# Optimization experiments

Hardware: AMD Instinct MI355X
Metric: run time of the kernel (lower is better)

Reference implementation:

```python
import jax, jax.numpy as jnp
import numpy as np

D_MODEL = 1024
N_HEADS = 16
D_FF = 4096
N_EXPERTS = 8
TOP_K = 2
BATCH = 2
SEQ = 2048
LN_EPS = 1e-5


def setup_inputs() -> dict:
    key = jax.random.key(0)
    ks = jax.random.split(key, 16)

    def w(k, shape, fan_in):
        return (jax.random.normal(k, shape, jnp.float32) / np.sqrt(fan_in)).astype(jnp.float32)

    D, F, E = D_MODEL, D_FF, N_EXPERTS
    return {
        "x": jax.random.normal(ks[0], (BATCH, SEQ, D), jnp.float32),
        "Wq": w(ks[1], (D, D), D), "bq": jnp.zeros((D,), jnp.float32),
        "Wk": w(ks[2], (D, D), D), "bk": jnp.zeros((D,), jnp.float32),
        "Wv": w(ks[3], (D, D), D), "bv": jnp.zeros((D,), jnp.float32),
        "Wo": w(ks[4], (D, D), D), "bo": jnp.zeros((D,), jnp.float32),
        "ln1_g": jnp.ones((D,), jnp.float32), "ln1_b": jnp.zeros((D,), jnp.float32),
        "gate_w": w(ks[5], (D, E), D), "gate_b": jnp.zeros((E,), jnp.float32),
        "W1": w(ks[6], (E, D, F), D), "b1": jnp.zeros((E, F), jnp.float32),
        "W2": w(ks[7], (E, F, D), F), "b2": jnp.zeros((E, D), jnp.float32),
        "ln3_g": jnp.ones((D,), jnp.float32), "ln3_b": jnp.zeros((D,), jnp.float32),
    }


def _layernorm(h, g, b):
    m = h.mean(-1, keepdims=True)
    v = ((h - m) ** 2).mean(-1, keepdims=True)
    return (h - m) * jax.lax.rsqrt(v + LN_EPS) * g + b


def _mha(x, Wq, bq, Wk, bk, Wv, bv, Wo, bo):
    B, S, D = x.shape
    H = N_HEADS
    dk = D // H
    q = (x @ Wq + bq).reshape(B, S, H, dk)
    k = (x @ Wk + bk).reshape(B, S, H, dk)
    v = (x @ Wv + bv).reshape(B, S, H, dk)
    scores = jnp.einsum("bqhd,bkhd->bhqk", q, k) / np.sqrt(dk)
    attn = jax.nn.softmax(scores, axis=-1)
    ctx = jnp.einsum("bhqk,bkhd->bqhd", attn, v).reshape(B, S, D)
    return ctx @ Wo + bo


def _moe(x, gate_w, gate_b, W1, b1, W2, b2):
    B, S, D = x.shape
    E = N_EXPERTS
    xf = x.reshape(-1, D)  # [T, D]
    logits = xf @ gate_w + gate_b  # [T, E]
    sc, idx = jax.lax.top_k(logits, TOP_K)
    sc = jax.nn.softmax(sc, axis=-1)  # softmax over the top-k scores only
    # combine weights per (token, expert): sum_k score_k * onehot(idx_k)
    comb = (jax.nn.one_hot(idx, E, dtype=xf.dtype) * sc[..., None]).sum(axis=1)  # [T, E]
    h = jnp.einsum("td,edf->tef", xf, W1) + b1  # [T, E, F]
    even = (jnp.arange(E) % 2 == 0)[None, :, None]
    a = jnp.where(even, jax.nn.gelu(h, approximate=False), jax.nn.silu(h))
    y = jnp.einsum("tef,efd->ted", a, W2) + b2  # [T, E, D]
    out = jnp.einsum("ted,te->td", y, comb)
    return out.reshape(B, S, D)


def reference(x, Wq, bq, Wk, bk, Wv, bv, Wo, bo, ln1_g, ln1_b,
              gate_w, gate_b, W1, b1, W2, b2, ln3_g, ln3_b):
    attn_out = _mha(x, Wq, bq, Wk, bk, Wv, bv, Wo, bo)
    x1 = _layernorm(x + attn_out, ln1_g, ln1_b)
    moe_out = _moe(x1, gate_w, gate_b, W1, b1, W2, b2)  # dropout: eval mode = identity
    return _layernorm(x1 + moe_out, ln3_g, ln3_b)
```

## Files before the change

kernel.cpp:

```cpp
#include <hip/hip_runtime.h>


typedef __attribute__((ext_vector_type(8))) short bf16x8;
typedef __attribute__((ext_vector_type(4))) float f32x4;

#define T_TOK 4096
#define DMODEL 1024
#define DFF 4096
#define NEXP 8
#define SEQ 2048
#define NSLOT 8192
#define NSLOT_PAD (8192+256)
#define LDS_STRIDE 72

__device__ __forceinline__ ushort f2b(float f) {
  union { float f; unsigned u; } v; v.f = f;
  unsigned r = (v.u + 0x7FFFu + ((v.u >> 16) & 1u)) >> 16;
  return (ushort)r;
}
__device__ __forceinline__ float b2f(ushort u) {
  union { unsigned u; float f; } v; v.u = ((unsigned)u) << 16; return v.f;
}


__global__ __launch_bounds__(256) void cvt_bf16(const float* __restrict__ in,
                                                ushort* __restrict__ out, long n,
                                                int* __restrict__ cnt) {
  if (blockIdx.x == 0 && threadIdx.x < 16) cnt[threadIdx.x] = 0;
  long i = ((long)blockIdx.x * 256 + threadIdx.x) * 4;
  if (i >= n) return;
  float4 v = *(const float4*)(in + i);
  ushort4 o; o.x = f2b(v.x); o.y = f2b(v.y); o.z = f2b(v.z); o.w = f2b(v.w);
  *(ushort4*)(out + i) = o;
}

__global__ __launch_bounds__(256) void wtrans(const float* __restrict__ in,
                                              ushort* __restrict__ out, int R, int C) {
  __shared__ float tile[64][65];
  long base = (long)blockIdx.z * R * C;
  int r0 = blockIdx.y * 64, c0 = blockIdx.x * 64;
  int t = threadIdx.x;
  int tr = t >> 4, tc = (t & 15) * 4;
#pragma unroll
  for (int i = 0; i < 4; i++) {
    float4 v = *(const float4*)(in + base + (long)(r0 + tr + i * 16) * C + c0 + tc);
    tile[tr + i * 16][tc + 0] = v.x; tile[tr + i * 16][tc + 1] = v.y;
    tile[tr + i * 16][tc + 2] = v.z; tile[tr + i * 16][tc + 3] = v.w;
  }
  __syncthreads();
#pragma unroll
  for (int i = 0; i < 4; i++) {
    int c = tr + i * 16, r = tc;
    ushort4 o;
    o.x = f2b(tile[r + 0][c]); o.y = f2b(tile[r + 1][c]);
    o.z = f2b(tile[r + 2][c]); o.w = f2b(tile[r + 3][c]);
    *(ushort4*)(out + base + (long)(c0 + c) * R + r0 + r) = o;
  }
}

__global__ __launch_bounds__(256) void vtrans(const ushort* __restrict__ Vb,
                                              ushort* __restrict__ Vt) {
  __shared__ ushort tile[64 * 72];
  int s0 = blockIdx.x * 64, h = blockIdx.y, b = blockIdx.z;
  int t = threadIdx.x;
  int chunk = t & 7;
#pragma unroll
  for (int rep = 0; rep < 2; rep++) {
    int row = (t >> 3) + rep * 32;
    *(uint4*)(tile + row * 72 + chunk * 8) =
        *(const uint4*)(Vb + (long)(b * SEQ + s0 + row) * DMODEL + h * 64 + chunk * 8);
  }
  __syncthreads();
#pragma unroll
  for (int rep = 0; rep < 2; rep++) {
    int idx = rep * 256 + t; int d = idx >> 3; int sc = (idx & 7) * 8;
    union { ushort u[8]; uint4 v; } tmp;
#pragma unroll
    for (int j = 0; j < 8; j++) tmp.u[j] = tile[(sc + j) * 72 + d];
    *(uint4*)(Vt + ((long)(b * 16 + h) * 64 + d) * SEQ + s0 + sc) = tmp.v;
  }
}


__device__ __forceinline__ void mainloop64(
    const ushort* a0, const ushort* a1, const ushort* a2, const ushort* a3,
    const ushort* b0, const ushort* b1, const ushort* b2, const ushort* b3,
    ushort* As, ushort* Bs, int K,
    int wm, int wn, int quad, int l15, f32x4 acc[4][4]) {
  const int t = threadIdx.x;
  const int rA = t >> 3, c8 = (t & 7) * 8;
  for (int k0 = 0; k0 < K; k0 += 64) {
    __syncthreads();
    *(uint4*)(As + (rA +  0) * LDS_STRIDE + c8) = *(const uint4*)(a0 + k0);
    *(uint4*)(As + (rA + 32) * LDS_STRIDE + c8) = *(const uint4*)(a1 + k0);
    *(uint4*)(As + (rA + 64) * LDS_STRIDE + c8) = *(const uint4*)(a2 + k0);
    *(uint4*)(As + (rA + 96) * LDS_STRIDE + c8) = *(const uint4*)(a3 + k0);
    *(uint4*)(Bs + (rA +  0) * LDS_STRIDE + c8) = *(const uint4*)(b0 + k0);
    *(uint4*)(Bs + (rA + 32) * LDS_STRIDE + c8) = *(const uint4*)(b1 + k0);
    *(uint4*)(Bs + (rA + 64) * LDS_STRIDE + c8) = *(const uint4*)(b2 + k0);
    *(uint4*)(Bs + (rA + 96) * LDS_STRIDE + c8) = *(const uint4*)(b3 + k0);
    __syncthreads();
#pragma unroll
    for (int kk = 0; kk < 64; kk += 32) {
      bf16x8 af[4], bfr[4];
#pragma unroll
      for (int i = 0; i < 4; i++)
        af[i] = *(const bf16x8*)(As + (wm + i * 16 + l15) * LDS_STRIDE + kk + quad * 8);
#pragma unroll
      for (int i = 0; i < 4; i++)
        bfr[i] = *(const bf16x8*)(Bs + (wn + i * 16 + l15) * LDS_STRIDE + kk + quad * 8);
#pragma unroll
      for (int mi = 0; mi < 4; mi++)
#pragma unroll
        for (int ni = 0; ni < 4; ni++)
          acc[mi][ni] = __builtin_amdgcn_mfma_f32_16x16x32_bf16(af[mi], bfr[ni], acc[mi][ni], 0, 0, 0);
    }
  }
}

__global__ __launch_bounds__(256, 2) void gemm_qkv(
    const ushort* __restrict__ A,
    const ushort* __restrict__ BtQ, const ushort* __restrict__ BtK, const ushort* __restrict__ BtV,
    const float* __restrict__ bq, const float* __restrict__ bk, const float* __restrict__ bv,
    ushort* __restrict__ oq, ushort* __restrict__ ok, ushort* __restrict__ ov) {
  __shared__ ushort As[128 * LDS_STRIDE], Bs[128 * LDS_STRIDE];
  int z = blockIdx.z;
  const ushort* Bt = (z == 0) ? BtQ : (z == 1) ? BtK : BtV;
  const float* bias = (z == 0) ? bq : (z == 1) ? bk : bv;
  ushort* outp = (z == 0) ? oq : (z == 1) ? ok : ov;
  float scale = (z == 0) ? 0.125f : 1.0f;
  const int m0 = blockIdx.y * 128, n0 = blockIdx.x * 128;
  const int t = threadIdx.x, w = t >> 6, lane = t & 63, quad = lane >> 4, l15 = lane & 15;
  const int wm = (w >> 1) * 64, wn = (w & 1) * 64;
  const int rA = t >> 3, c8 = (t & 7) * 8;
  const ushort* a0 = A + (long)(m0 + rA) * DMODEL + c8;
  const ushort* b0 = Bt + (long)(n0 + rA) * DMODEL + c8;
  f32x4 acc[4][4];
  f32x4 zv = {0.f, 0.f, 0.f, 0.f};
  for (int i = 0; i < 4; i++) for (int j = 0; j < 4; j++) acc[i][j] = zv;
  mainloop64(a0, a0 + 32 * DMODEL, a0 + 64 * DMODEL, a0 + 96 * DMODEL,
             b0, b0 + 32 * DMODEL, b0 + 64 * DMODEL, b0 + 96 * DMODEL,
             As, Bs, DMODEL, wm, wn, quad, l15, acc);
#pragma unroll
  for (int mi = 0; mi < 4; mi++)
#pragma unroll
    for (int ni = 0; ni < 4; ni++) {
      int row = m0 + wm + mi * 16 + quad * 4;
      int col = n0 + wn + ni * 16 + l15;
      float bb = bias[col];
#pragma unroll
      for (int r = 0; r < 4; r++)
        outp[(long)(row + r) * DMODEL + col] = f2b((acc[mi][ni][r] + bb) * scale);
    }
}

__global__ __launch_bounds__(256, 2) void gemm_oproj(
    const ushort* __restrict__ A, const ushort* __restrict__ Bt,
    const float* __restrict__ bias, const float* __restrict__ resid,
    float* __restrict__ outf) {
  __shared__ ushort As[128 * LDS_STRIDE], Bs[128 * LDS_STRIDE];
  const int m0 = blockIdx.y * 128, n0 = blockIdx.x * 128;
  const int t = threadIdx.x, w = t >> 6, lane = t & 63, quad = lane >> 4, l15 = lane & 15;
  const int wm = (w >> 1) * 64, wn = (w & 1) * 64;
  const int rA = t >> 3, c8 = (t & 7) * 8;
  const ushort* a0 = A + (long)(m0 + rA) * DMODEL + c8;
  const ushort* b0 = Bt + (long)(n0 + rA) * DMODEL + c8;
  f32x4 acc[4][4];
  f32x4 zv = {0.f, 0.f, 0.f, 0.f};
  for (int i = 0; i < 4; i++) for (int j = 0; j < 4; j++) acc[i][j] = zv;
  mainloop64(a0, a0 + 32 * DMODEL, a0 + 64 * DMODEL, a0 + 96 * DMODEL,
             b0, b0 + 32 * DMODEL, b0 + 64 * DMODEL, b0 + 96 * DMODEL,
             As, Bs, DMODEL, wm, wn, quad, l15, acc);
#pragma unroll
  for (int mi = 0; mi < 4; mi++)
#pragma unroll
    for (int ni = 0; ni < 4; ni++) {
      int row = m0 + wm + mi * 16 + quad * 4;
      int col = n0 + wn + ni * 16 + l15;
      float bb = bias[col];
#pragma unroll
      for (int r = 0; r < 4; r++) {
        long idx = (long)(row + r) * DMODEL + col;
        outf[idx] = acc[mi][ni][r] + bb + resid[idx];
      }
    }
}

__global__ __launch_bounds__(256, 2) void gemm_moe(
    int mode, const ushort* __restrict__ Abase, const int* __restrict__ slot_token,
    const ushort* __restrict__ WT, const float* __restrict__ biasE,
    ushort* __restrict__ outp, int K, int N,
    const int* __restrict__ tab_e, const int* __restrict__ tab_r0,
    const int* __restrict__ tab_end, const int* __restrict__ nmb) {
  int mb = blockIdx.y;
  if (mb >= *nmb) return;
  __shared__ ushort As[128 * LDS_STRIDE], Bs[128 * LDS_STRIDE];
  int e = tab_e[mb], r0 = tab_r0[mb], rend = tab_end[mb];
  const int t = threadIdx.x, w = t >> 6, lane = t & 63, quad = lane >> 4, l15 = lane & 15;
  const int wm = (w >> 1) * 64, wn = (w & 1) * 64;
  const int rA = t >> 3, c8 = (t & 7) * 8;
  const int n0 = blockIdx.x * 128;
  const ushort* ap[4];
#pragma unroll
  for (int j = 0; j < 4; j++) {
    int r = r0 + rA + 32 * j;
    if (mode == 2) {
      int ci = r < rend ? r : rend - 1;
      ap[j] = Abase + (long)slot_token[ci] * K + c8;
    } else {
      ap[j] = Abase + (long)r * K + c8;
    }
  }
  const ushort* Bt = WT + (long)e * K * N;
  const ushort* b0 = Bt + (long)(n0 + rA) * K + c8;
  f32x4 acc[4][4];
  f32x4 zv = {0.f, 0.f, 0.f, 0.f};
  for (int i = 0; i < 4; i++) for (int j = 0; j < 4; j++) acc[i][j] = zv;
  mainloop64(ap[0], ap[1], ap[2], ap[3],
             b0, b0 + (long)32 * K, b0 + (long)64 * K, b0 + (long)96 * K,
             As, Bs, K, wm, wn, quad, l15, acc);
  const float* bb = biasE + (long)e * N;
  bool odd = (e & 1) != 0;
#pragma unroll
  for (int mi = 0; mi < 4; mi++)
#pragma unroll
    for (int ni = 0; ni < 4; ni++) {
      int col = n0 + wn + ni * 16 + l15;
      float bv = bb[col];
#pragma unroll
      for (int r = 0; r < 4; r++) {
        int slot = r0 + wm + mi * 16 + quad * 4 + r;
        if (slot < rend) {
          float v = acc[mi][ni][r] + bv;
          if (mode == 2)
            v = odd ? (v / (1.f + __expf(-v)))
                    : (0.5f * v * (1.f + erff(v * 0.70710678118f)));
          outp[(long)slot * N + col] = f2b(v);
        }
      }
    }
}

__global__ __launch_bounds__(256, 2) void flash_attn(
    const ushort* __restrict__ Qb, const ushort* __restrict__ Kb,
    const ushort* __restrict__ Vt, ushort* __restrict__ ctx) {
  __shared__ ushort QP[128 * 72];
  __shared__ ushort Ks[64 * 72];
  __shared__ ushort Vs[64 * 72];
  const int t = threadIdx.x, w = t >> 6, lane = t & 63, quad = lane >> 4, l15 = lane & 15;
  const int q0 = blockIdx.x * 128, bh = blockIdx.y, b = bh >> 4, h = bh & 15;
  {
    int chunk = t & 7, hcol = h * 64 + chunk * 8;
#pragma unroll
    for (int rep = 0; rep < 4; rep++) {
      int row = (t >> 3) + rep * 32;
      *(uint4*)(QP + row * 72 + chunk * 8) =
          *(const uint4*)(Qb + (long)(b * SEQ + q0 + row) * DMODEL + hcol);
    }
  }
  __syncthreads();
  bf16x8 qf[2][2];
#pragma unroll
  for (int rt = 0; rt < 2; rt++)
#pragma unroll
    for (int kc = 0; kc < 2; kc++)
      qf[rt][kc] = *(const bf16x8*)(QP + (w * 32 + rt * 16 + l15) * 72 + kc * 32 + quad * 8);

  f32x4 O[2][4];
  f32x4 zv = {0.f, 0.f, 0.f, 0.f};
  float m_r[2][4], l_r[2][4];
#pragma unroll
  for (int rt = 0; rt < 2; rt++)
#pragma unroll
    for (int i = 0; i < 4; i++) { O[rt][i] = zv; m_r[rt][i] = -1e30f; l_r[rt][i] = 0.f; }

  for (int kv0 = 0; kv0 < SEQ; kv0 += 64) {
    __syncthreads();
    {
      int chunk = t & 7, hcol = h * 64 + chunk * 8;
#pragma unroll
      for (int rep = 0; rep < 2; rep++) {
        int row = (t >> 3) + rep * 32;
        *(uint4*)(Ks + row * 72 + chunk * 8) =
            *(const uint4*)(Kb + (long)(b * SEQ + kv0 + row) * DMODEL + hcol);
        *(uint4*)(Vs + row * 72 + chunk * 8) =
            *(const uint4*)(Vt + ((long)bh * 64 + row) * SEQ + kv0 + chunk * 8);
      }
    }
    __syncthreads();
    f32x4 S[2][4];
#pragma unroll
    for (int ct = 0; ct < 4; ct++) {
      bf16x8 kf0 = *(const bf16x8*)(Ks + (ct * 16 + l15) * 72 + quad * 8);
      bf16x8 kf1 = *(const bf16x8*)(Ks + (ct * 16 + l15) * 72 + 32 + quad * 8);
#pragma unroll
      for (int rt = 0; rt < 2; rt++) {
        f32x4 s = zv;
        s = __builtin_amdgcn_mfma_f32_16x16x32_bf16(qf[rt][0], kf0, s, 0, 0, 0);
        s = __builtin_amdgcn_mfma_f32_16x16x32_bf16(qf[rt][1], kf1, s, 0, 0, 0);
        S[rt][ct] = s;
      }
    }
#pragma unroll
    for (int rt = 0; rt < 2; rt++) {
#pragma unroll
      for (int r = 0; r < 4; r++) {
        float mx = fmaxf(fmaxf(S[rt][0][r], S[rt][1][r]), fmaxf(S[rt][2][r], S[rt][3][r]));
        mx = fmaxf(mx, __shfl_xor(mx, 1));
        mx = fmaxf(mx, __shfl_xor(mx, 2));
        mx = fmaxf(mx, __shfl_xor(mx, 4));
        mx = fmaxf(mx, __shfl_xor(mx, 8));
        float nm = fmaxf(m_r[rt][r], mx);
        float alpha = __expf(m_r[rt][r] - nm);
        m_r[rt][r] = nm;
        float p0 = __expf(S[rt][0][r] - nm), p1 = __expf(S[rt][1][r] - nm);
        float p2 = __expf(S[rt][2][r] - nm), p3 = __expf(S[rt][3][r] - nm);
        float rs = p0 + p1 + p2 + p3;
        rs += __shfl_xor(rs, 1); rs += __shfl_xor(rs, 2);
        rs += __shfl_xor(rs, 4); rs += __shfl_xor(rs, 8);
        l_r[rt][r] = l_r[rt][r] * alpha + rs;
#pragma unroll
        for (int dt = 0; dt < 4; dt++) O[rt][dt][r] *= alpha;
        int prow = (w * 32 + rt * 16 + quad * 4 + r) * 72;
        QP[prow + 0 * 16 + l15] = f2b(p0);
        QP[prow + 1 * 16 + l15] = f2b(p1);
        QP[prow + 2 * 16 + l15] = f2b(p2);
        QP[prow + 3 * 16 + l15] = f2b(p3);
      }
    }
    bf16x8 pf[2][2];
#pragma unroll
    for (int rt = 0; rt < 2; rt++)
#pragma unroll
      for (int ks = 0; ks < 2; ks++)
        pf[rt][ks] = *(const bf16x8*)(QP + (w * 32 + rt * 16 + l15) * 72 + ks * 32 + quad * 8);
#pragma unroll
    for (int dt = 0; dt < 4; dt++) {
      bf16x8 vf0 = *(const bf16x8*)(Vs + (dt * 16 + l15) * 72 + quad * 8);
      bf16x8 vf1 = *(const bf16x8*)(Vs + (dt * 16 + l15) * 72 + 32 + quad * 8);
#pragma unroll
      for (int rt = 0; rt < 2; rt++) {
        O[rt][dt] = __builtin_amdgcn_mfma_f32_16x16x32_bf16(pf[rt][0], vf0, O[rt][dt], 0, 0, 0);
        O[rt][dt] = __builtin_amdgcn_mfma_f32_16x16x32_bf16(pf[rt][1], vf1, O[rt][dt], 0, 0, 0);
      }
    }
  }
#pragma unroll
  for (int rt = 0; rt < 2; rt++)
#pragma unroll
    for (int r = 0; r < 4; r++) {
      float inv = 1.f / l_r[rt][r];
      int row = b * SEQ + q0 + w * 32 + rt * 16 + quad * 4 + r;
#pragma unroll
      for (int dt = 0; dt < 4; dt++)
        ctx[(long)row * DMODEL + h * 64 + dt * 16 + l15] = f2b(O[rt][dt][r] * inv);
    }
}


__device__ __forceinline__ float block_sum(float v, float* red) {
#pragma unroll
  for (int off = 32; off; off >>= 1) v += __shfl_down(v, off);
  int w = threadIdx.x >> 6;
  __syncthreads();
  if ((threadIdx.x & 63) == 0) red[w] = v;
  __syncthreads();
  return red[0] + red[1] + red[2] + red[3];
}

__global__ __launch_bounds__(256) void ln1_gate(const float* __restrict__ in,
    const float* __restrict__ g, const float* __restrict__ bb,
    const float* __restrict__ gw, const float* __restrict__ gb,
    float* __restrict__ outf, ushort* __restrict__ outh,
    int* __restrict__ top2i, float* __restrict__ top2s, int* __restrict__ cnt) {
  __shared__ float red[4];
  __shared__ float red8[4][8];
  long row = blockIdx.x;
  int t = threadIdx.x, w = t >> 6, lane = t & 63;
  float4 v = *(const float4*)(in + row * DMODEL + t * 4);
  float s = block_sum(v.x + v.y + v.z + v.w, red);
  float mean = s * (1.0f / DMODEL);
  float d0 = v.x - mean, d1 = v.y - mean, d2 = v.z - mean, d3 = v.w - mean;
  float sq = block_sum(d0 * d0 + d1 * d1 + d2 * d2 + d3 * d3, red);
  float rstd = rsqrtf(sq * (1.0f / DMODEL) + 1e-5f);
  float4 gg = *(const float4*)(g + t * 4);
  float4 bv = *(const float4*)(bb + t * 4);
  float o0 = d0 * rstd * gg.x + bv.x, o1 = d1 * rstd * gg.y + bv.y;
  float o2 = d2 * rstd * gg.z + bv.z, o3 = d3 * rstd * gg.w + bv.w;
  float4 of; of.x = o0; of.y = o1; of.z = o2; of.w = o3;
  *(float4*)(outf + row * DMODEL + t * 4) = of;
  ushort4 oh; oh.x = f2b(o0); oh.y = f2b(o1); oh.z = f2b(o2); oh.w = f2b(o3);
  *(ushort4*)(outh + row * DMODEL + t * 4) = oh;
  float a[8];
  {
    const float* gr = gw + (long)(t * 4) * 8;
    float4 w0 = *(const float4*)(gr +  0), w1 = *(const float4*)(gr +  4);
    float4 w2 = *(const float4*)(gr +  8), w3 = *(const float4*)(gr + 12);
    float4 w4 = *(const float4*)(gr + 16), w5 = *(const float4*)(gr + 20);
    float4 w6 = *(const float4*)(gr + 24), w7 = *(const float4*)(gr + 28);
    a[0] = o0 * w0.x + o1 * w2.x + o2 * w4.x + o3 * w6.x;
    a[1] = o0 * w0.y + o1 * w2.y + o2 * w4.y + o3 * w6.y;
    a[2] = o0 * w0.z + o1 * w2.z + o2 * w4.z + o3 * w6.z;
    a[3] = o0 * w0.w + o1 * w2.w + o2 * w4.w + o3 * w6.w;
    a[4] = o0 * w1.x + o1 * w3.x + o2 * w5.x + o3 * w7.x;
    a[5] = o0 * w1.y + o1 * w3.y + o2 * w5.y + o3 * w7.y;
    a[6] = o0 * w1.z + o1 * w3.z + o2 * w5.z + o3 * w7.z;
    a[7] = o0 * w1.w + o1 * w3.w + o2 * w5.w + o3 * w7.w;
  }
#pragma unroll
  for (int off = 32; off; off >>= 1)
#pragma unroll
    for (int e = 0; e < 8; e++) a[e] += __shfl_down(a[e], off);
  if (lane == 0) {
#pragma unroll
    for (int e = 0; e < 8; e++) red8[w][e] = a[e];
  }
  __syncthreads();
  if (t == 0) {
    float L[8];
#pragma unroll
    for (int e = 0; e < 8; e++)
      L[e] = red8[0][e] + red8[1][e] + red8[2][e] + red8[3][e] + gb[e];
    int e0 = 0; float v0 = L[0];
#pragma unroll
    for (int e = 1; e < 8; e++) if (L[e] > v0) { v0 = L[e]; e0 = e; }
    int e1 = -1; float v1 = -1e30f;
#pragma unroll
    for (int e = 0; e < 8; e++) if (e != e0 && L[e] > v1) { v1 = L[e]; e1 = e; }
    float q = __expf(v1 - v0);
    float inv = 1.f / (1.f + q);
    top2i[2 * row] = e0; top2i[2 * row + 1] = e1;
    top2s[2 * row] = inv; top2s[2 * row + 1] = q * inv;
    atomicAdd(&cnt[e0], 1); atomicAdd(&cnt[e1], 1);
  }
}

__global__ void build_tables(const int* __restrict__ cnt, int* __restrict__ off,
                             int* __restrict__ tab_e, int* __restrict__ tab_r0,
                             int* __restrict__ tab_end, int* __restrict__ nmb) {
  if (threadIdx.x == 0 && blockIdx.x == 0) {
    int o = 0, m = 0;
    for (int e = 0; e < NEXP; e++) {
      off[e] = o;
      int c = cnt[e];
      for (int j = 0; j * 128 < c; j++) { tab_e[m] = e; tab_r0[m] = o + j * 128; tab_end[m] = o + c; m++; }
      o += c;
    }
    off[NEXP] = o;
    *nmb = m;
  }
}

__global__ __launch_bounds__(256) void scatter_slots(const int* __restrict__ top2i,
    const float* __restrict__ top2s, const int* __restrict__ off, int* __restrict__ fill,
    int* __restrict__ slot_token, float* __restrict__ slot_scale, int* __restrict__ pos) {
  int t = blockIdx.x * 256 + threadIdx.x;
  if (t >= T_TOK) return;
#pragma unroll
  for (int k = 0; k < 2; k++) {
    int e = top2i[2 * t + k];
    int p = off[e] + atomicAdd(&fill[e], 1);
    slot_token[p] = t;
    slot_scale[p] = top2s[2 * t + k];
    pos[2 * t + k] = p;
  }
}

__global__ __launch_bounds__(256) void combine_ln3(const float* __restrict__ x1,
    const ushort* __restrict__ ybuf, const int* __restrict__ pos,
    const float* __restrict__ sscale, const float* __restrict__ g,
    const float* __restrict__ bb, float* __restrict__ outp) {
  __shared__ float red[4];
  long row = blockIdx.x;
  int t = threadIdx.x;
  int p0 = pos[2 * row], p1 = pos[2 * row + 1];
  float s0 = sscale[p0], s1 = sscale[p1];
  float4 xv = *(const float4*)(x1 + row * DMODEL + t * 4);
  ushort4 y0 = *(const ushort4*)(ybuf + (long)p0 * DMODEL + t * 4);
  ushort4 y1 = *(const ushort4*)(ybuf + (long)p1 * DMODEL + t * 4);
  float v0 = xv.x + s0 * b2f(y0.x) + s1 * b2f(y1.x);
  float v1 = xv.y + s0 * b2f(y0.y) + s1 * b2f(y1.y);
  float v2 = xv.z + s0 * b2f(y0.z) + s1 * b2f(y1.z);
  float v3 = xv.w + s0 * b2f(y0.w) + s1 * b2f(y1.w);
  float s = block_sum(v0 + v1 + v2 + v3, red);
  float mean = s * (1.0f / DMODEL);
  float d0 = v0 - mean, d1 = v1 - mean, d2 = v2 - mean, d3 = v3 - mean;
  float sq = block_sum(d0 * d0 + d1 * d1 + d2 * d2 + d3 * d3, red);
  float rstd = rsqrtf(sq * (1.0f / DMODEL) + 1e-5f);
  float4 gg = *(const float4*)(g + t * 4);
  float4 bv = *(const float4*)(bb + t * 4);
  float4 of;
  of.x = d0 * rstd * gg.x + bv.x; of.y = d1 * rstd * gg.y + bv.y;
  of.z = d2 * rstd * gg.z + bv.z; of.w = d3 * rstd * gg.w + bv.w;
  *(float4*)(outp + row * DMODEL + t * 4) = of;
}


extern "C" void kernel_launch(void* const* d_in, const int* in_sizes, int n_in,
                              void* d_out, int out_size, void* d_ws, size_t ws_size,
                              hipStream_t stream) {
  (void)in_sizes; (void)n_in; (void)out_size;
  const float* x    = (const float*)d_in[0];
  const float* Wq   = (const float*)d_in[1];
  const float* bq   = (const float*)d_in[2];
  const float* Wk   = (const float*)d_in[3];
  const float* bk   = (const float*)d_in[4];
  const float* Wv   = (const float*)d_in[5];
  const float* bv   = (const float*)d_in[6];
  const float* Wo   = (const float*)d_in[7];
  const float* bo   = (const float*)d_in[8];
  const float* ln1g = (const float*)d_in[9];
  const float* ln1b = (const float*)d_in[10];
  const float* gw   = (const float*)d_in[11];
  const float* gb   = (const float*)d_in[12];
  const float* W1   = (const float*)d_in[13];
  const float* b1   = (const float*)d_in[14];
  const float* W2   = (const float*)d_in[15];
  const float* b2   = (const float*)d_in[16];
  const float* ln3g = (const float*)d_in[17];
  const float* ln3b = (const float*)d_in[18];
  float* outp = (float*)d_out;

  char* ws = (char*)d_ws;
  size_t o = 0;
  auto alloc = [&](size_t b) { size_t r = o; o = (o + b + 255) & ~(size_t)255; return r; };
  const long T = T_TOK, D = DMODEL, F = DFF;
  size_t wqT_o = alloc(D * D * 2), wkT_o = alloc(D * D * 2);
  size_t wvT_o = alloc(D * D * 2), woT_o = alloc(D * D * 2);
  size_t w1T_o = alloc((size_t)NEXP * D * F * 2);
  size_t w2T_o = alloc((size_t)NEXP * D * F * 2);
  size_t xb_o  = alloc(T * D * 2);
  size_t x1f_o = alloc(T * D * 4);
  size_t x1b_o = alloc(T * D * 2);
  size_t yb_o  = alloc((size_t)NSLOT * D * 2);
  size_t ab_o  = alloc((size_t)NSLOT_PAD * F * 2);
  size_t cnt_o = alloc(64);
  size_t off_o = alloc(64);
  size_t nmb_o = alloc(16);
  size_t tabe_o = alloc(80 * 4), tabr_o = alloc(80 * 4), tabn_o = alloc(80 * 4);
  size_t t2i_o = alloc((size_t)NSLOT * 4), t2s_o = alloc((size_t)NSLOT * 4);
  size_t st_o = alloc((size_t)NSLOT * 4), ss_o = alloc((size_t)NSLOT * 4);
  size_t pos_o = alloc((size_t)NSLOT * 4);
  if (o > ws_size) return;

  ushort* wqT = (ushort*)(ws + wqT_o); ushort* wkT = (ushort*)(ws + wkT_o);
  ushort* wvT = (ushort*)(ws + wvT_o); ushort* woT = (ushort*)(ws + woT_o);
  ushort* w1T = (ushort*)(ws + w1T_o); ushort* w2T = (ushort*)(ws + w2T_o);
  ushort* xb  = (ushort*)(ws + xb_o);
  float*  x1f = (float*)(ws + x1f_o);
  ushort* x1b = (ushort*)(ws + x1b_o);
  ushort* ybuf = (ushort*)(ws + yb_o);
  ushort* abuf = (ushort*)(ws + ab_o);
  ushort* qb = abuf;
  ushort* kb = qb + T * D;
  ushort* vb = kb + T * D;
  ushort* vt = vb + T * D;
  ushort* ctx = vt + T * D;
  int* cnt = (int*)(ws + cnt_o); int* fill = cnt + 8;
  int* offe = (int*)(ws + off_o);
  int* nmb = (int*)(ws + nmb_o);
  int* tab_e = (int*)(ws + tabe_o); int* tab_r0 = (int*)(ws + tabr_o);
  int* tab_end = (int*)(ws + tabn_o);
  int* top2i = (int*)(ws + t2i_o); float* top2s = (float*)(ws + t2s_o);
  int* slot_token = (int*)(ws + st_o); float* slot_scale = (float*)(ws + ss_o);
  int* pos = (int*)(ws + pos_o);

  hipLaunchKernelGGL(cvt_bf16, dim3((T * D) / 1024), dim3(256), 0, stream, x, xb, T * D, cnt);
  hipLaunchKernelGGL(wtrans, dim3(16, 16, 1), dim3(256), 0, stream, Wq, wqT, (int)D, (int)D);
  hipLaunchKernelGGL(wtrans, dim3(16, 16, 1), dim3(256), 0, stream, Wk, wkT, (int)D, (int)D);
  hipLaunchKernelGGL(wtrans, dim3(16, 16, 1), dim3(256), 0, stream, Wv, wvT, (int)D, (int)D);
  hipLaunchKernelGGL(wtrans, dim3(16, 16, 1), dim3(256), 0, stream, Wo, woT, (int)D, (int)D);
  hipLaunchKernelGGL(wtrans, dim3(64, 16, 8), dim3(256), 0, stream, W1, w1T, (int)D, (int)F);
  hipLaunchKernelGGL(wtrans, dim3(16, 64, 8), dim3(256), 0, stream, W2, w2T, (int)F, (int)D);
  hipLaunchKernelGGL(gemm_qkv, dim3(8, 32, 3), dim3(256), 0, stream,
                     xb, wqT, wkT, wvT, bq, bk, bv, qb, kb, vb);
  hipLaunchKernelGGL(vtrans, dim3(32, 16, 2), dim3(256), 0, stream, vb, vt);
  hipLaunchKernelGGL(flash_attn, dim3(16, 32), dim3(256), 0, stream, qb, kb, vt, ctx);
  hipLaunchKernelGGL(gemm_oproj, dim3(8, 32), dim3(256), 0, stream, ctx, woT, bo, x, x1f);
  hipLaunchKernelGGL(ln1_gate, dim3(T), dim3(256), 0, stream,
                     x1f, ln1g, ln1b, gw, gb, x1f, x1b, top2i, top2s, cnt);
  hipLaunchKernelGGL(build_tables, dim3(1), dim3(64), 0, stream, cnt, offe, tab_e, tab_r0, tab_end, nmb);
  hipLaunchKernelGGL(scatter_slots, dim3(T / 256), dim3(256), 0, stream,
                     top2i, top2s, offe, fill, slot_token, slot_scale, pos);
  hipLaunchKernelGGL(gemm_moe, dim3(32, 72), dim3(256), 0, stream,
                     2, x1b, slot_token, w1T, b1, abuf, (int)D, (int)F,
                     tab_e, tab_r0, tab_end, nmb);
  hipLaunchKernelGGL(gemm_moe, dim3(8, 72), dim3(256), 0, stream,
                     3, abuf, slot_token, w2T, b2, ybuf, (int)F, (int)D,
                     tab_e, tab_r0, tab_end, nmb);
  hipLaunchKernelGGL(combine_ln3, dim3(T), dim3(256), 0, stream,
                     x1f, ybuf, pos, slot_scale, ln3g, ln3b, outp);
}
```

Before: 1.041 ms.

## Prefetch GEMM tiles into registers, use direct-to-LDS loads, shrink attention query tile

The GEMM mainloop now loads the next K tile from global memory into registers while the current tile is computed, and is used for the QKV and MoE GEMMs. The output projection instead uses global_load_lds to copy straight into an unpadded LDS layout. Flash attention now handles 64 query rows per block instead of 128, doubling the grid and raising the occupancy hint to 4 blocks per CU. These changes aim to hide global load latency and improve occupancy, at the cost of extra registers, possible LDS bank conflicts from the unpadded layout, and twice the K/V reloads in attention.

```diff
diff --git a/kernel.cpp b/kernel.cpp
--- a/kernel.cpp
+++ b/kernel.cpp
@@ -3,6 +3,9 @@
 
 typedef __attribute__((ext_vector_type(8))) short bf16x8;
 typedef __attribute__((ext_vector_type(4))) float f32x4;
+
+typedef const __attribute__((address_space(1))) unsigned int* gas_p;
+typedef __attribute__((address_space(3))) unsigned int* las_p;
 
 #define T_TOK 4096
 #define DMODEL 1024
@@ -20,6 +23,10 @@
 }
 __device__ __forceinline__ float b2f(ushort u) {
   union { unsigned u; float f; } v; v.u = ((unsigned)u) << 16; return v.f;
+}
+
+__device__ __forceinline__ void gload16(const ushort* g, ushort* lds) {
+  __builtin_amdgcn_global_load_lds((gas_p)g, (las_p)lds, 16, 0, 0);
 }
 
 
@@ -82,23 +89,34 @@
 }
 
 
-__device__ __forceinline__ void mainloop64(
+__device__ __forceinline__ void mainloop64_reg(
     const ushort* a0, const ushort* a1, const ushort* a2, const ushort* a3,
     const ushort* b0, const ushort* b1, const ushort* b2, const ushort* b3,
     ushort* As, ushort* Bs, int K,
     int wm, int wn, int quad, int l15, f32x4 acc[4][4]) {
   const int t = threadIdx.x;
   const int rA = t >> 3, c8 = (t & 7) * 8;
+  uint4 ra0 = *(const uint4*)a0, ra1 = *(const uint4*)a1;
+  uint4 ra2 = *(const uint4*)a2, ra3 = *(const uint4*)a3;
+  uint4 rb0 = *(const uint4*)b0, rb1 = *(const uint4*)b1;
+  uint4 rb2 = *(const uint4*)b2, rb3 = *(const uint4*)b3;
   for (int k0 = 0; k0 < K; k0 += 64) {
     __syncthreads();
-    *(uint4*)(As + (rA +  0) * LDS_STRIDE + c8) = *(const uint4*)(a0 + k0);
-    *(uint4*)(As + (rA + 32) * LDS_STRIDE + c8) = *(const uint4*)(a1 + k0);
-    *(uint4*)(As + (rA + 64) * LDS_STRIDE + c8) = *(const uint4*)(a2 + k0);
-    *(uint4*)(As + (rA + 96) * LDS_STRIDE + c8) = *(const uint4*)(a3 + k0);
-    *(uint4*)(Bs + (rA +  0) * LDS_STRIDE + c8) = *(const uint4*)(b0 + k0);
-    *(uint4*)(Bs + (rA + 32) * LDS_STRIDE + c8) = *(const uint4*)(b1 + k0);
-    *(uint4*)(Bs + (rA + 64) * LDS_STRIDE + c8) = *(const uint4*)(b2 + k0);
-    *(uint4*)(Bs + (rA + 96) * LDS_STRIDE + c8) = *(const uint4*)(b3 + k0);
+    *(uint4*)(As + (rA +  0) * LDS_STRIDE + c8) = ra0;
+    *(uint4*)(As + (rA + 32) * LDS_STRIDE + c8) = ra1;
+    *(uint4*)(As + (rA + 64) * LDS_STRIDE + c8) = ra2;
+    *(uint4*)(As + (rA + 96) * LDS_STRIDE + c8) = ra3;
+    *(uint4*)(Bs + (rA +  0) * LDS_STRIDE + c8) = rb0;
+    *(uint4*)(Bs + (rA + 32) * LDS_STRIDE + c8) = rb1;
+    *(uint4*)(Bs + (rA + 64) * LDS_STRIDE + c8) = rb2;
+    *(uint4*)(Bs + (rA + 96) * LDS_STRIDE + c8) = rb3;
+    int kn = k0 + 64;
+    if (kn < K) {
+      ra0 = *(const uint4*)(a0 + kn); ra1 = *(const uint4*)(a1 + kn);
+      ra2 = *(const uint4*)(a2 + kn); ra3 = *(const uint4*)(a3 + kn);
+      rb0 = *(const uint4*)(b0 + kn); rb1 = *(const uint4*)(b1 + kn);
+      rb2 = *(const uint4*)(b2 + kn); rb3 = *(const uint4*)(b3 + kn);
+    }
     __syncthreads();
 #pragma unroll
     for (int kk = 0; kk < 64; kk += 32) {
@@ -109,6 +127,44 @@
 #pragma unroll
       for (int i = 0; i < 4; i++)
         bfr[i] = *(const bf16x8*)(Bs + (wn + i * 16 + l15) * LDS_STRIDE + kk + quad * 8);
+#pragma unroll
+      for (int mi = 0; mi < 4; mi++)
+#pragma unroll
+        for (int ni = 0; ni < 4; ni++)
+          acc[mi][ni] = __builtin_amdgcn_mfma_f32_16x16x32_bf16(af[mi], bfr[ni], acc[mi][ni], 0, 0, 0);
+    }
+  }
+}
+
+
+__device__ __forceinline__ void mainloop64_lds(
+    const ushort* a0, const ushort* a1, const ushort* a2, const ushort* a3,
+    const ushort* b0, const ushort* b1, const ushort* b2, const ushort* b3,
+    ushort* As, ushort* Bs, int K,
+    int wm, int wn, int quad, int l15, f32x4 acc[4][4]) {
+  const int w = threadIdx.x >> 6;
+  ushort* Asw = As + w * 8 * 64;
+  ushort* Bsw = Bs + w * 8 * 64;
+  for (int k0 = 0; k0 < K; k0 += 64) {
+    __syncthreads();
+    gload16(a0 + k0, Asw + 0 * 64);
+    gload16(a1 + k0, Asw + 32 * 64);
+    gload16(a2 + k0, Asw + 64 * 64);
+    gload16(a3 + k0, Asw + 96 * 64);
+    gload16(b0 + k0, Bsw + 0 * 64);
+    gload16(b1 + k0, Bsw + 32 * 64);
+    gload16(b2 + k0, Bsw + 64 * 64);
+    gload16(b3 + k0, Bsw + 96 * 64);
+    __syncthreads();
+#pragma unroll
+    for (int kk = 0; kk < 64; kk += 32) {
+      bf16x8 af[4], bfr[4];
+#pragma unroll
+      for (int i = 0; i < 4; i++)
+        af[i] = *(const bf16x8*)(As + (wm + i * 16 + l15) * 64 + kk + quad * 8);
+#pragma unroll
+      for (int i = 0; i < 4; i++)
+        bfr[i] = *(const bf16x8*)(Bs + (wn + i * 16 + l15) * 64 + kk + quad * 8);
 #pragma unroll
       for (int mi = 0; mi < 4; mi++)
 #pragma unroll
@@ -138,9 +194,9 @@
   f32x4 acc[4][4];
   f32x4 zv = {0.f, 0.f, 0.f, 0.f};
   for (int i = 0; i < 4; i++) for (int j = 0; j < 4; j++) acc[i][j] = zv;
-  mainloop64(a0, a0 + 32 * DMODEL, a0 + 64 * DMODEL, a0 + 96 * DMODEL,
-             b0, b0 + 32 * DMODEL, b0 + 64 * DMODEL, b0 + 96 * DMODEL,
-             As, Bs, DMODEL, wm, wn, quad, l15, acc);
+  mainloop64_reg(a0, a0 + 32 * DMODEL, a0 + 64 * DMODEL, a0 + 96 * DMODEL,
+                 b0, b0 + 32 * DMODEL, b0 + 64 * DMODEL, b0 + 96 * DMODEL,
+                 As, Bs, DMODEL, wm, wn, quad, l15, acc);
 #pragma unroll
   for (int mi = 0; mi < 4; mi++)
 #pragma unroll
@@ -158,7 +214,7 @@
     const ushort* __restrict__ A, const ushort* __restrict__ Bt,
     const float* __restrict__ bias, const float* __restrict__ resid,
     float* __restrict__ outf) {
-  __shared__ ushort As[128 * LDS_STRIDE], Bs[128 * LDS_STRIDE];
+  __shared__ ushort As[128 * 64], Bs[128 * 64];
   const int m0 = blockIdx.y * 128, n0 = blockIdx.x * 128;
   const int t = threadIdx.x, w = t >> 6, lane = t & 63, quad = lane >> 4, l15 = lane & 15;
   const int wm = (w >> 1) * 64, wn = (w & 1) * 64;
@@ -168,9 +224,9 @@
   f32x4 acc[4][4];
   f32x4 zv = {0.f, 0.f, 0.f, 0.f};
   for (int i = 0; i < 4; i++) for (int j = 0; j < 4; j++) acc[i][j] = zv;
-  mainloop64(a0, a0 + 32 * DMODEL, a0 + 64 * DMODEL, a0 + 96 * DMODEL,
-             b0, b0 + 32 * DMODEL, b0 + 64 * DMODEL, b0 + 96 * DMODEL,
-             As, Bs, DMODEL, wm, wn, quad, l15, acc);
+  mainloop64_lds(a0, a0 + 32 * DMODEL, a0 + 64 * DMODEL, a0 + 96 * DMODEL,
+                 b0, b0 + 32 * DMODEL, b0 + 64 * DMODEL, b0 + 96 * DMODEL,
+                 As, Bs, DMODEL, wm, wn, quad, l15, acc);
 #pragma unroll
   for (int mi = 0; mi < 4; mi++)
 #pragma unroll
@@ -216,9 +272,9 @@
   f32x4 acc[4][4];
   f32x4 zv = {0.f, 0.f, 0.f, 0.f};
   for (int i = 0; i < 4; i++) for (int j = 0; j < 4; j++) acc[i][j] = zv;
-  mainloop64(ap[0], ap[1], ap[2], ap[3],
-             b0, b0 + (long)32 * K, b0 + (long)64 * K, b0 + (long)96 * K,
-             As, Bs, K, wm, wn, quad, l15, acc);
+  mainloop64_reg(ap[0], ap[1], ap[2], ap[3],
+                 b0, b0 + (long)32 * K, b0 + (long)64 * K, b0 + (long)96 * K,
+                 As, Bs, K, wm, wn, quad, l15, acc);
   const float* bb = biasE + (long)e * N;
   bool odd = (e & 1) != 0;
 #pragma unroll
@@ -241,38 +297,34 @@
     }
 }
 
-__global__ __launch_bounds__(256, 2) void flash_attn(
+__global__ __launch_bounds__(256, 4) void flash_attn(
     const ushort* __restrict__ Qb, const ushort* __restrict__ Kb,
     const ushort* __restrict__ Vt, ushort* __restrict__ ctx) {
-  __shared__ ushort QP[128 * 72];
+  __shared__ ushort QP[64 * 72];
   __shared__ ushort Ks[64 * 72];
   __shared__ ushort Vs[64 * 72];
   const int t = threadIdx.x, w = t >> 6, lane = t & 63, quad = lane >> 4, l15 = lane & 15;
-  const int q0 = blockIdx.x * 128, bh = blockIdx.y, b = bh >> 4, h = bh & 15;
+  const int q0 = blockIdx.x * 64, bh = blockIdx.y, b = bh >> 4, h = bh & 15;
   {
     int chunk = t & 7, hcol = h * 64 + chunk * 8;
 #pragma unroll
-    for (int rep = 0; rep < 4; rep++) {
+    for (int rep = 0; rep < 2; rep++) {
       int row = (t >> 3) + rep * 32;
       *(uint4*)(QP + row * 72 + chunk * 8) =
           *(const uint4*)(Qb + (long)(b * SEQ + q0 + row) * DMODEL + hcol);
     }
   }
   __syncthreads();
-  bf16x8 qf[2][2];
-#pragma unroll
-  for (int rt = 0; rt < 2; rt++)
-#pragma unroll
-    for (int kc = 0; kc < 2; kc++)
-      qf[rt][kc] = *(const bf16x8*)(QP + (w * 32 + rt * 16 + l15) * 72 + kc * 32 + quad * 8);
-
-  f32x4 O[2][4];
+  bf16x8 qf[2];
+#pragma unroll
+  for (int kc = 0; kc < 2; kc++)
+    qf[kc] = *(const bf16x8*)(QP + (w * 16 + l15) * 72 + kc * 32 + quad * 8);
+
+  f32x4 O[4];
   f32x4 zv = {0.f, 0.f, 0.f, 0.f};
-  float m_r[2][4], l_r[2][4];
-#pragma unroll
-  for (int rt = 0; rt < 2; rt++)
-#pragma unroll
-    for (int i = 0; i < 4; i++) { O[rt][i] = zv; m_r[rt][i] = -1e30f; l_r[rt][i] = 0.f; }
+  float m_r[4], l_r[4];
+#pragma unroll
+  for (int i = 0; i < 4; i++) { O[i] = zv; m_r[i] = -1e30f; l_r[i] = 0.f; }
 
   for (int kv0 = 0; kv0 < SEQ; kv0 += 64) {
     __syncthreads();
@@ -288,73 +340,60 @@
       }
     }
     __syncthreads();
-    f32x4 S[2][4];
+    f32x4 S[4];
 #pragma unroll
     for (int ct = 0; ct < 4; ct++) {
       bf16x8 kf0 = *(const bf16x8*)(Ks + (ct * 16 + l15) * 72 + quad * 8);
       bf16x8 kf1 = *(const bf16x8*)(Ks + (ct * 16 + l15) * 72 + 32 + quad * 8);
-#pragma unroll
-      for (int rt = 0; rt < 2; rt++) {
-        f32x4 s = zv;
-        s = __builtin_amdgcn_mfma_f32_16x16x32_bf16(qf[rt][0], kf0, s, 0, 0, 0);
-        s = __builtin_amdgcn_mfma_f32_16x16x32_bf16(qf[rt][1], kf1, s, 0, 0, 0);
-        S[rt][ct] = s;
-      }
-    }
-#pragma unroll
-    for (int rt = 0; rt < 2; rt++) {
-#pragma unroll
-      for (int r = 0; r < 4; r++) {
-        float mx = fmaxf(fmaxf(S[rt][0][r], S[rt][1][r]), fmaxf(S[rt][2][r], S[rt][3][r]));
-        mx = fmaxf(mx, __shfl_xor(mx, 1));
-        mx = fmaxf(mx, __shfl_xor(mx, 2));
-        mx = fmaxf(mx, __shfl_xor(mx, 4));
-        mx = fmaxf(mx, __shfl_xor(mx, 8));
-        float nm = fmaxf(m_r[rt][r], mx);
-        float alpha = __expf(m_r[rt][r] - nm);
-        m_r[rt][r] = nm;
-        float p0 = __expf(S[rt][0][r] - nm), p1 = __expf(S[rt][1][r] - nm);
-        float p2 = __expf(S[rt][2][r] - nm), p3 = __expf(S[rt][3][r] - nm);
-        float rs = p0 + p1 + p2 + p3;
-        rs += __shfl_xor(rs, 1); rs += __shfl_xor(rs, 2);
-        rs += __shfl_xor(rs, 4); rs += __shfl_xor(rs, 8);
-        l_r[rt][r] = l_r[rt][r] * alpha + rs;
-#pragma unroll
-        for (int dt = 0; dt < 4; dt++) O[rt][dt][r] *= alpha;
-        int prow = (w * 32 + rt * 16 + quad * 4 + r) * 72;
-        QP[prow + 0 * 16 + l15] = f2b(p0);
-        QP[prow + 1 * 16 + l15] = f2b(p1);
-        QP[prow + 2 * 16 + l15] = f2b(p2);
-        QP[prow + 3 * 16 + l15] = f2b(p3);
-      }
-    }
-    bf16x8 pf[2][2];
-#pragma unroll
-    for (int rt = 0; rt < 2; rt++)
-#pragma unroll
-      for (int ks = 0; ks < 2; ks++)
-        pf[rt][ks] = *(const bf16x8*)(QP + (w * 32 + rt * 16 + l15) * 72 + ks * 32 + quad * 8);
+      f32x4 s = zv;
+      s = __builtin_amdgcn_mfma_f32_16x16x32_bf16(qf[0], kf0, s, 0, 0, 0);
+      s = __builtin_amdgcn_mfma_f32_16x16x32_bf16(qf[1], kf1, s, 0, 0, 0);
+      S[ct] = s;
+    }
+#pragma unroll
+    for (int r = 0; r < 4; r++) {
+      float mx = fmaxf(fmaxf(S[0][r], S[1][r]), fmaxf(S[2][r], S[3][r]));
+      mx = fmaxf(mx, __shfl_xor(mx, 1));
+      mx = fmaxf(mx, __shfl_xor(mx, 2));
+      mx = fmaxf(mx, __shfl_xor(mx, 4));
+      mx = fmaxf(mx, __shfl_xor(mx, 8));
+      float nm = fmaxf(m_r[r], mx);
+      float alpha = __expf(m_r[r] - nm);
+      m_r[r] = nm;
+      float p0 = __expf(S[0][r] - nm), p1 = __expf(S[1][r] - nm);
+      float p2 = __expf(S[2][r] - nm), p3 = __expf(S[3][r] - nm);
+      float rs = p0 + p1 + p2 + p3;
+      rs += __shfl_xor(rs, 1); rs += __shfl_xor(rs, 2);
+      rs += __shfl_xor(rs, 4); rs += __shfl_xor(rs, 8);
+      l_r[r] = l_r[r] * alpha + rs;
+#pragma unroll
+      for (int dt = 0; dt < 4; dt++) O[dt][r] *= alpha;
+      int prow = (w * 16 + quad * 4 + r) * 72;
+      QP[prow + 0 * 16 + l15] = f2b(p0);
+      QP[prow + 1 * 16 + l15] = f2b(p1);
+      QP[prow + 2 * 16 + l15] = f2b(p2);
+      QP[prow + 3 * 16 + l15] = f2b(p3);
+    }
+    bf16x8 pf[2];
+#pragma unroll
+    for (int ks = 0; ks < 2; ks++)
+      pf[ks] = *(const bf16x8*)(QP + (w * 16 + l15) * 72 + ks * 32 + quad * 8);
 #pragma unroll
     for (int dt = 0; dt < 4; dt++) {
       bf16x8 vf0 = *(const bf16x8*)(Vs + (dt * 16 + l15) * 72 + quad * 8);
       bf16x8 vf1 = *(const bf16x8*)(Vs + (dt * 16 + l15) * 72 + 32 + quad * 8);
-#pragma unroll
-      for (int rt = 0; rt < 2; rt++) {
-        O[rt][dt] = __builtin_amdgcn_mfma_f32_16x16x32_bf16(pf[rt][0], vf0, O[rt][dt], 0, 0, 0);
-        O[rt][dt] = __builtin_amdgcn_mfma_f32_16x16x32_bf16(pf[rt][1], vf1, O[rt][dt], 0, 0, 0);
-      }
-    }
-  }
-#pragma unroll
-  for (int rt = 0; rt < 2; rt++)
-#pragma unroll
-    for (int r = 0; r < 4; r++) {
-      float inv = 1.f / l_r[rt][r];
-      int row = b * SEQ + q0 + w * 32 + rt * 16 + quad * 4 + r;
-#pragma unroll
-      for (int dt = 0; dt < 4; dt++)
-        ctx[(long)row * DMODEL + h * 64 + dt * 16 + l15] = f2b(O[rt][dt][r] * inv);
-    }
+      O[dt] = __builtin_amdgcn_mfma_f32_16x16x32_bf16(pf[0], vf0, O[dt], 0, 0, 0);
+      O[dt] = __builtin_amdgcn_mfma_f32_16x16x32_bf16(pf[1], vf1, O[dt], 0, 0, 0);
+    }
+  }
+#pragma unroll
+  for (int r = 0; r < 4; r++) {
+    float inv = 1.f / l_r[r];
+    int row = b * SEQ + q0 + w * 16 + quad * 4 + r;
+#pragma unroll
+    for (int dt = 0; dt < 4; dt++)
+      ctx[(long)row * DMODEL + h * 64 + dt * 16 + l15] = f2b(O[dt][r] * inv);
+  }
 }
 
 
@@ -575,7 +614,7 @@
   hipLaunchKernelGGL(gemm_qkv, dim3(8, 32, 3), dim3(256), 0, stream,
                      xb, wqT, wkT, wvT, bq, bk, bv, qb, kb, vb);
   hipLaunchKernelGGL(vtrans, dim3(32, 16, 2), dim3(256), 0, stream, vb, vt);
-  hipLaunchKernelGGL(flash_attn, dim3(16, 32), dim3(256), 0, stream, qb, kb, vt, ctx);
+  hipLaunchKernelGGL(flash_attn, dim3(32, 32), dim3(256), 0, stream, qb, kb, vt, ctx);
   hipLaunchKernelGGL(gemm_oproj, dim3(8, 32), dim3(256), 0, stream, ctx, woT, bo, x, x1f);
   hipLaunchKernelGGL(ln1_gate, dim3(T), dim3(256), 0, stream,
                      x1f, ln1g, ln1b, gw, gb, x1f, x1b, top2i, top2s, cnt);
```

New measurement: 940.8 us. 1.11x faster.
